# Kernel optimization log

Hardware: AMD Instinct MI355X
Metric: run time of the kernel (lower is better)

Reference implementation:

```python
import jax, jax.numpy as jnp
import numpy as np

N_NODES, N_EDGES, MAX_LEN, OB_DIM, HEADS = 4000, 64000, 64, 4, 1
IN_CH = MAX_LEN * OB_DIM          # 256
OUT_CH = MAX_LEN * OB_DIM         # 256
PE_DIM = 16                        # map_weights (heads*16) + p_t (16) cat -> 32


def setup_inputs() -> dict:
    key = jax.random.key(0)
    ks = jax.random.split(key, 8)
    x = jax.random.normal(ks[0], (N_NODES, IN_CH), dtype=jnp.float32)
    p_t = jax.random.normal(ks[1], (MAX_LEN, PE_DIM), dtype=jnp.float32)
    edge_index = jax.random.randint(ks[2], (2, N_EDGES), 0, N_NODES, dtype=jnp.int64)
    edge_weights = jax.random.uniform(ks[3], (N_EDGES,), dtype=jnp.float32)
    # learned params (torch Linear stored transposed: y = x @ W + b)
    s = 1.0 / np.sqrt(IN_CH)
    W_value = jax.random.uniform(ks[4], (IN_CH, HEADS * OUT_CH), jnp.float32, -s, s)
    b_value = jnp.zeros((HEADS * OUT_CH,), jnp.float32)
    W_inc = jax.random.uniform(ks[5], (IN_CH, HEADS * OUT_CH * 8), jnp.float32, -s, s)
    b_inc = jnp.zeros((HEADS * OUT_CH * 8,), jnp.float32)
    map_weights = jax.random.normal(ks[6], (N_NODES, HEADS * 16), jnp.float32) * 0.1
    return {"x": x, "p_t": p_t, "edge_index": edge_index, "edge_weights": edge_weights,
            "W_value": W_value, "b_value": b_value, "W_inc": W_inc, "b_inc": b_inc,
            "map_weights": map_weights}


def _segment_softmax(vals, index, num_segments):
    # PyG softmax: per-destination-segment, columnwise, with 1e-16 in denom
    seg_max = jax.ops.segment_max(vals, index, num_segments=num_segments)
    ex = jnp.exp(vals - seg_max[index])
    seg_sum = jax.ops.segment_sum(ex, index, num_segments=num_segments)
    return ex / (seg_sum[index] + 1e-16)


def reference(x, p_t, edge_index, edge_weights, W_value, b_value, W_inc, b_inc, map_weights):
    N = x.shape[0]
    E = edge_index.shape[1]
    L = p_t.shape[0]                      # n_step
    dst = edge_index[1]
    x_i = x[dst]                          # [E, IN_CH] gather of target-node feats
    # beta scoring (use_beta=True path)
    h_W = (x_i @ W_inc + b_inc).reshape(E, L, 32)
    w_v = map_weights[dst][:, None, :]    # [E, 1, 16]
    aa = jnp.concatenate([jnp.broadcast_to(w_v, (E, L, w_v.shape[-1])),
                          jnp.broadcast_to(p_t[None], (E, L, p_t.shape[-1]))], axis=-1)
    beta = jnp.mean(h_W * aa, axis=-1)    # [E, L]
    gamma = beta * edge_weights[:, None]  # [E, L]
    gamma = jnp.repeat(gamma, OB_DIM, axis=-1)   # [E, L*OB_DIM] == [E, HEADS*OUT_CH]
    all_edge_weights = jnp.mean(gamma, axis=1)   # [E]
    K = E // 2
    _, top_idx = jax.lax.top_k(all_edge_weights, K)
    gamma = gamma[top_idx]
    ei = edge_index[:, top_idx]
    index = ei[0]                          # faithful: original reassigns index = edge_index[0]
    x_i = x_i[top_idx]
    # segment softmax + weighted value aggregation
    gamma = _segment_softmax(gamma, index, N)
    out = jax.nn.relu(x_i @ W_value + b_value).reshape(K, HEADS, OUT_CH)
    out = out * gamma.reshape(K, HEADS, OUT_CH)
    out = jax.ops.segment_sum(out, index, num_segments=N)   # scatter-add aggregate
    return out.reshape(N, HEADS * OUT_CH)   # concat=True
```

## Files before the change

kernel.cpp:

```cpp
#include <hip/hip_runtime.h>
#include <stdint.h>

#define NN   4000
#define EE   64000
#define KSEL 32000
#define CAP  64

typedef __attribute__((ext_vector_type(8))) short bf16x8;
typedef __attribute__((ext_vector_type(4))) float f32x4;

static constexpr size_t O_HIST1 = 0;
static constexpr size_t O_HIST2 = 16384;
static constexpr size_t O_META  = 32768;
static constexpr size_t O_CNT   = 33024;
static constexpr size_t ZERO_BYTES = 49024;
static constexpr size_t O_BUCK  = 49024;
static constexpr size_t O_KEYS  = 1073024;
static constexpr size_t O_CAND  = 1585024;
static constexpr size_t O_CAND2 = 1841024;
static constexpr size_t O_MEANB = 2097024;
static constexpr size_t O_BMAT  = 2129024;
static constexpr size_t O_V     = 3153024;
static constexpr size_t O_WALLT = 5201024;
static constexpr size_t O_WVT   = 5758080;
static constexpr size_t O_WST   = 5889152;
static constexpr size_t O_BS1   = 5923968;
static constexpr size_t O_CB    = 5924096;
static constexpr size_t O_CONST = 5924352;

__device__ __forceinline__ unsigned short f2b(float f) {
  union { float f; unsigned u; } v; v.f = f;
  const unsigned r = v.u + 0x7fffu + ((v.u >> 16) & 1u);
  return (unsigned short)(r >> 16);
}
__device__ __forceinline__ float b2f(unsigned short b) {
  return __uint_as_float(((unsigned)b) << 16);
}
__device__ __forceinline__ bf16x8 ld_cvt8(const float* __restrict__ p) {
  const float4 fa = *(const float4*)p;
  const float4 fb = *(const float4*)(p + 4);
  bf16x8 r;
  r[0] = (short)f2b(fa.x); r[1] = (short)f2b(fa.y);
  r[2] = (short)f2b(fa.z); r[3] = (short)f2b(fa.w);
  r[4] = (short)f2b(fb.x); r[5] = (short)f2b(fb.y);
  r[6] = (short)f2b(fb.z); r[7] = (short)f2b(fb.w);
  return r;
}

__device__ __forceinline__ void block_select(const unsigned* __restrict__ hist,
                                             unsigned target, unsigned* sh,
                                             unsigned& pbin, unsigned& rem) {
  const int t = threadIdx.x;
  unsigned h[16];
  unsigned s = 0;
#pragma unroll
  for (int b = 0; b < 16; ++b) { h[b] = hist[t * 16 + b]; s += h[b]; }
  sh[t] = s;
  __syncthreads();
  for (int off = 1; off < 256; off <<= 1) {
    const unsigned a = (t + off < 256) ? sh[t + off] : 0u;
    __syncthreads();
    sh[t] += a;
    __syncthreads();
  }
  const unsigned mysuf = sh[t];
  const unsigned sufnext = (t < 255) ? sh[t + 1] : 0u;
  __syncthreads();
  if (mysuf >= target && sufnext < target) {
    unsigned cum = sufnext;
#pragma unroll
    for (int b = 15; b >= 0; --b) {
      const unsigned hv = h[b];
      if (cum + hv >= target) { sh[256] = (unsigned)(t * 16 + b); sh[257] = target - cum; break; }
      cum += hv;
    }
  }
  __syncthreads();
  pbin = sh[256]; rem = sh[257];
  __syncthreads();
}

__global__ void rk_prep(const float* __restrict__ W_inc, const float* __restrict__ p_t,
                        const float* __restrict__ b_inc, const float* __restrict__ W_value,
                        unsigned short* __restrict__ Wallt, unsigned short* __restrict__ Wvt,
                        double* __restrict__ WsT,
                        double* __restrict__ bs1, float* __restrict__ cb,
                        double* __restrict__ consts, unsigned* __restrict__ zws) {
  const int i = blockIdx.x;
  const int l = threadIdx.x;
  const int gid = i * 64 + l;
  if (gid < (int)(ZERO_BYTES / 4)) zws[gid] = 0u;
  __shared__ double sred[64];
  const int base = i * 2048 + l * 32;
#pragma unroll
  for (int c = 0; c < 16; ++c)
    Wallt[(size_t)(l * 16 + c) * 256 + i] = f2b(W_inc[base + c]);
  double accP = 0.0;
#pragma unroll
  for (int c = 0; c < 16; ++c)
    accP += (double)W_inc[base + 16 + c] * (double)p_t[l * 16 + c];
  Wallt[(size_t)(1024 + l) * 256 + i] = f2b((float)accP);
#pragma unroll
  for (int j = 0; j < 4; ++j)
    Wvt[(size_t)(l * 4 + j) * 256 + i] = f2b(W_value[i * 256 + l * 4 + j]);
  sred[l] = accP;
  __syncthreads();
  if (l == 0) {
    double s = 0.0;
    for (int j = 0; j < 64; ++j) s += sred[j];
    WsT[16 * 256 + i] = s;
  }
  if (l < 16) {
    double s = 0.0;
    for (int l2 = 0; l2 < 64; ++l2) s += (double)W_inc[i * 2048 + l2 * 32 + l];
    WsT[l * 256 + i] = s;
  }
  if (i == 0) {
    __syncthreads();
    if (l < 16) {
      double s = 0.0;
      for (int l2 = 0; l2 < 64; ++l2) s += (double)b_inc[l2 * 32 + l];
      bs1[l] = s;
    }
    double cbv = 0.0;
#pragma unroll
    for (int c = 0; c < 16; ++c)
      cbv += (double)p_t[l * 16 + c] * (double)b_inc[l * 32 + 16 + c];
    cb[l] = (float)cbv;
    sred[l] = cbv;
    __syncthreads();
    if (l == 0) {
      double s = 0.0;
      for (int j = 0; j < 64; ++j) s += sred[j];
      consts[0] = s;
    }
  }
}

__global__ __launch_bounds__(256) void rk_mbv(
    const float* __restrict__ x, const float* __restrict__ mw,
    const double* __restrict__ WsT,
    const double* __restrict__ bs1, const double* __restrict__ consts,
    double* __restrict__ meanB,
    const unsigned short* __restrict__ Wallt, const unsigned short* __restrict__ Wvt,
    const float* __restrict__ b_inc, const float* __restrict__ cb,
    const float* __restrict__ b_value,
    float* __restrict__ Bmat, unsigned short* __restrict__ V) {
  __shared__ double wst[17 * 256];
  const int bid = blockIdx.x;
  const int t = threadIdx.x;
  if (bid < 250) {
#pragma unroll
    for (int j = 0; j < 17; ++j) wst[j * 256 + t] = WsT[j * 256 + t];
    __syncthreads();
    const int lt = t & 63;
    const int w = t >> 6;
#pragma unroll
    for (int nn = 0; nn < 4; ++nn) {
      const int n = bid * 16 + w * 4 + nn;
      double mwv[16];
#pragma unroll
      for (int c = 0; c < 16; ++c) mwv[c] = (double)mw[n * 16 + c];
      double acc = 0.0;
#pragma unroll
      for (int rep = 0; rep < 4; ++rep) {
        const int i = lt + rep * 64;
        double weff = wst[16 * 256 + i];
#pragma unroll
        for (int c = 0; c < 16; ++c) weff += mwv[c] * wst[c * 256 + i];
        acc += (double)x[n * 256 + i] * weff;
      }
      for (int off = 32; off > 0; off >>= 1) acc += __shfl_down(acc, off, 64);
      if (lt == 0) {
        double s = acc + consts[0];
#pragma unroll
        for (int c = 0; c < 16; ++c) s += mwv[c] * bs1[c];
        meanB[n] = s * (1.0 / 2048.0);
      }
    }
  } else {
    const int b2 = bid - 250;
    const int wv = t >> 6, lane = t & 63;
    const int lr = lane & 15, kg = lane >> 4;
    const int n0 = (b2 % 125) * 32;
    const int by = b2 / 125;
    const int l0 = by * 16;
    const int c0 = by * 64 + wv * 16;
    f32x4 acc[2][5] = {};
    f32x4 accv[2] = {};
    const float* ax0 = x + (size_t)(n0 + lr) * 256 + kg * 8;
    const float* ax1 = ax0 + 16 * 256;
    const unsigned short* bp[5];
#pragma unroll
    for (int j = 0; j < 4; ++j)
      bp[j] = Wallt + (size_t)((l0 + wv * 4 + j) * 16 + lr) * 256 + kg * 8;
    bp[4] = Wallt + (size_t)(1024 + l0 + lr) * 256 + kg * 8;
    const unsigned short* bpv = Wvt + (size_t)(c0 + lr) * 256 + kg * 8;
#pragma unroll
    for (int kk = 0; kk < 8; ++kk) {
      const bf16x8 a0 = ld_cvt8(ax0 + kk * 32);
      const bf16x8 a1 = ld_cvt8(ax1 + kk * 32);
#pragma unroll
      for (int j = 0; j < 5; ++j) {
        const bf16x8 b = *(const bf16x8*)(bp[j] + kk * 32);
        acc[0][j] = __builtin_amdgcn_mfma_f32_16x16x32_bf16(a0, b, acc[0][j], 0, 0, 0);
        acc[1][j] = __builtin_amdgcn_mfma_f32_16x16x32_bf16(a1, b, acc[1][j], 0, 0, 0);
      }
      const bf16x8 bv = *(const bf16x8*)(bpv + kk * 32);
      accv[0] = __builtin_amdgcn_mfma_f32_16x16x32_bf16(a0, bv, accv[0], 0, 0, 0);
      accv[1] = __builtin_amdgcn_mfma_f32_16x16x32_bf16(a1, bv, accv[1], 0, 0, 0);
    }
    const int c = lr, rg = kg;
#pragma unroll
    for (int rt = 0; rt < 2; ++rt) {
      const int rbase = n0 + rt * 16 + rg * 4;
      float mwv[4];
#pragma unroll
      for (int r = 0; r < 4; ++r) mwv[r] = mw[(rbase + r) * 16 + c];
#pragma unroll
      for (int j = 0; j < 4; ++j) {
        const int lj = l0 + wv * 4 + j;
        const float bi = b_inc[lj * 32 + c];
        const float cbl = cb[lj];
#pragma unroll
        for (int r = 0; r < 4; ++r) {
          float prod = (acc[rt][j][r] + bi) * mwv[r];
#pragma unroll
          for (int off = 1; off < 16; off <<= 1) prod += __shfl_xor(prod, off, 64);
          const float c2 = __shfl(acc[rt][4][r], (lane & 48) | (wv * 4 + j), 64);
          if (c == 0) Bmat[(rbase + r) * 64 + lj] = (prod + c2 + cbl) * (1.0f / 32.0f);
        }
      }
    }
    const float bv = b_value[c0 + c];
#pragma unroll
    for (int rt = 0; rt < 2; ++rt)
#pragma unroll
      for (int r = 0; r < 4; ++r) {
        const float val = fmaxf(accv[rt][r] + bv, 0.f);
        V[(size_t)(n0 + rt * 16 + rg * 4 + r) * 256 + c0 + c] = f2b(val);
      }
  }
}

__global__ void rk_keys(const int* __restrict__ ei, const float* __restrict__ ew,
                        const double* __restrict__ meanB,
                        unsigned long long* __restrict__ keys, unsigned* __restrict__ hist1) {
  __shared__ unsigned lh[4096];
  const int t = threadIdx.x;
#pragma unroll
  for (int i = 0; i < 16; ++i) lh[t + i * 256] = 0u;
  __syncthreads();
  const int e = blockIdx.x * 256 + t;
  const int dst = ei[EE + e];
  const double aew = (double)ew[e] * meanB[dst];
  const unsigned long long b = (unsigned long long)__double_as_longlong(aew);
  const unsigned long long s = (b & 0x8000000000000000ull) ? ~b : (b | 0x8000000000000000ull);
  keys[e] = s;
  atomicAdd(&lh[(unsigned)(s >> 52)], 1u);
  __syncthreads();
#pragma unroll
  for (int i = 0; i < 16; ++i) {
    const unsigned v = lh[t + i * 256];
    if (v) atomicAdd(&hist1[t + i * 256], v);
  }
}

__global__ void rk_mark1(const unsigned long long* __restrict__ keys, const int* __restrict__ ei,
                         unsigned* __restrict__ meta, int* __restrict__ cand,
                         unsigned* __restrict__ cnt, int* __restrict__ bucket,
                         const unsigned* __restrict__ hist1, unsigned* __restrict__ hist2) {
  __shared__ unsigned sh[258];
  unsigned p1, m1;
  block_select(hist1, (unsigned)KSEL, sh, p1, m1);
  if (blockIdx.x == 0 && threadIdx.x == 0) { meta[0] = p1; meta[1] = m1; }
  const int e = blockIdx.x * 256 + threadIdx.x;
  const unsigned long long k = keys[e];
  const unsigned b12 = (unsigned)(k >> 52);
  if (b12 > p1) {
    const int src = ei[e];
    const unsigned pos = atomicAdd(&cnt[src], 1u);
    bucket[src * CAP + pos] = e;
  } else if (b12 == p1) {
    const unsigned pos = atomicAdd(&meta[2], 1u);
    cand[pos] = e;
    atomicAdd(&hist2[(unsigned)(k >> 40) & 0xFFFu], 1u);
  }
}

__global__ __launch_bounds__(1024) void rk_m2t(
    const unsigned long long* __restrict__ keys, const int* __restrict__ ei,
    unsigned* __restrict__ meta, const int* __restrict__ cand,
    int* __restrict__ cand2, unsigned* __restrict__ cnt, int* __restrict__ bucket,
    const unsigned* __restrict__ hist2) {
  __shared__ unsigned suf[1024];
  __shared__ unsigned sp[2];
  const int t = threadIdx.x;
  const unsigned m1 = meta[1];
  unsigned h[4];
  unsigned s = 0;
#pragma unroll
  for (int b = 0; b < 4; ++b) { h[b] = hist2[t * 4 + b]; s += h[b]; }
  suf[t] = s;
  __syncthreads();
  for (int off = 1; off < 1024; off <<= 1) {
    const unsigned a = (t + off < 1024) ? suf[t + off] : 0u;
    __syncthreads();
    suf[t] += a;
    __syncthreads();
  }
  const unsigned mysuf = suf[t];
  const unsigned sufnext = (t < 1023) ? suf[t + 1] : 0u;
  if (mysuf >= m1 && sufnext < m1) {
    unsigned cum = sufnext;
#pragma unroll
    for (int b = 3; b >= 0; --b) {
      const unsigned hv = h[b];
      if (cum + hv >= m1) { sp[0] = (unsigned)(t * 4 + b); sp[1] = m1 - cum; break; }
      cum += hv;
    }
  }
  __syncthreads();
  const unsigned p2 = sp[0], m2 = sp[1];
  const int C1 = (int)meta[2];
  for (int i = t; i < C1; i += 1024) {
    const int e = cand[i];
    const unsigned d12 = (unsigned)(keys[e] >> 40) & 0xFFFu;
    if (d12 > p2) {
      const int src = ei[e];
      const unsigned pos = atomicAdd(&cnt[src], 1u);
      bucket[src * CAP + pos] = e;
    } else if (d12 == p2) {
      const unsigned pos = atomicAdd(&meta[3], 1u);
      cand2[pos] = e;
    }
  }
  __threadfence();
  __syncthreads();
  const int C2 = (int)__hip_atomic_load(&meta[3], __ATOMIC_ACQUIRE, __HIP_MEMORY_SCOPE_AGENT);
  for (int i = t; i < C2; i += 1024) {
    const int e_i = cand2[i];
    const unsigned long long k_i = keys[e_i];
    int r = 0;
    for (int j = 0; j < C2; ++j) {
      const int e_j = cand2[j];
      const unsigned long long k_j = keys[e_j];
      if (k_j > k_i || (k_j == k_i && e_j < e_i)) ++r;
    }
    if (r < (int)m2) {
      const int src = ei[e_i];
      const unsigned pos = atomicAdd(&cnt[src], 1u);
      bucket[src * CAP + pos] = e_i;
    }
  }
}

__global__ void rk_out(const int* __restrict__ ei, const float* __restrict__ ew,
                       const unsigned* __restrict__ cnt, const int* __restrict__ bucket,
                       const float* __restrict__ Bmat, const unsigned short* __restrict__ V,
                       float* __restrict__ out) {
  const int n = blockIdx.x;
  const int t = threadIdx.x;
  const int l = t >> 2;
  __shared__ int   sdst[CAP];
  __shared__ float sew[CAP];
  const unsigned d = cnt[n];
  if (t < (int)d) {
    const int e = bucket[n * CAP + t];
    sdst[t] = ei[EE + e];
    sew[t] = ew[e];
  }
  __syncthreads();
  float s = 0.f, acc = 0.f;
  for (unsigned i = 0; i < d; ++i) {
    const int dst = sdst[i];
    const float p = __expf(Bmat[dst * 64 + l] * sew[i]);
    s += p;
    acc += p * b2f(V[(size_t)dst * 256 + t]);
  }
  out[(size_t)n * 256 + t] = acc / (s + 1e-16f);
}

extern "C" void kernel_launch(void* const* d_in, const int* in_sizes, int n_in,
                              void* d_out, int out_size, void* d_ws, size_t ws_size,
                              hipStream_t stream) {
  const float* x       = (const float*)d_in[0];
  const float* p_t     = (const float*)d_in[1];
  const int*   ei      = (const int*)d_in[2];
  const float* ew      = (const float*)d_in[3];
  const float* W_value = (const float*)d_in[4];
  const float* b_value = (const float*)d_in[5];
  const float* W_inc   = (const float*)d_in[6];
  const float* b_inc   = (const float*)d_in[7];
  const float* mw      = (const float*)d_in[8];
  float* out = (float*)d_out;
  char* ws = (char*)d_ws;

  unsigned*           hist1 = (unsigned*)(ws + O_HIST1);
  unsigned*           hist2 = (unsigned*)(ws + O_HIST2);
  unsigned*           meta  = (unsigned*)(ws + O_META);
  unsigned*           cnt   = (unsigned*)(ws + O_CNT);
  int*                buck  = (int*)(ws + O_BUCK);
  unsigned long long* keys  = (unsigned long long*)(ws + O_KEYS);
  int*                cand  = (int*)(ws + O_CAND);
  int*                cand2 = (int*)(ws + O_CAND2);
  double*             meanB = (double*)(ws + O_MEANB);
  float*              Bmat  = (float*)(ws + O_BMAT);
  unsigned short*     V     = (unsigned short*)(ws + O_V);
  unsigned short*     Wallt = (unsigned short*)(ws + O_WALLT);
  unsigned short*     Wvt   = (unsigned short*)(ws + O_WVT);
  double*             WsT   = (double*)(ws + O_WST);
  double*             bs1   = (double*)(ws + O_BS1);
  float*              cb    = (float*)(ws + O_CB);
  double*             cst   = (double*)(ws + O_CONST);

  rk_prep<<<256, 64, 0, stream>>>(W_inc, p_t, b_inc, W_value, Wallt, Wvt,
                                  WsT, bs1, cb, cst, (unsigned*)ws);
  rk_mbv<<<750, 256, 0, stream>>>(x, mw, WsT, bs1, cst, meanB,
                                  Wallt, Wvt, b_inc, cb, b_value, Bmat, V);
  rk_keys<<<250, 256, 0, stream>>>(ei, ew, meanB, keys, hist1);
  rk_mark1<<<250, 256, 0, stream>>>(keys, ei, meta, cand, cnt, buck, hist1, hist2);
  rk_m2t<<<1, 1024, 0, stream>>>(keys, ei, meta, cand, cand2, cnt, buck, hist2);
  rk_out<<<NN, 256, 0, stream>>>(ei, ew, cnt, buck, Bmat, V, out);
}
```

Before: 74.63 us.

## Split fused meanB/Bmat kernel into two separate launches

The combined rk_mbv kernel, which branched by block index between an FP64 meanB reduction and an MFMA GEMM for Bmat and V, is split into two kernels. The meanB kernel now handles one node per wave across 1000 blocks instead of four per wave, preloads x, and breaks the 16-term FP64 dot product into four independent accumulators to shorten the dependency chain. Separating the kernels lets each be compiled with its own register and LDS budget rather than the union of both paths. The cost is an extra launch and serialization between the two kernels, which previously ran concurrently within one grid.

New measurement: 76.79 us. 2.9% more time.

```diff
diff --git a/kernel.cpp b/kernel.cpp
--- a/kernel.cpp
+++ b/kernel.cpp
@@ -137,110 +137,114 @@
   }
 }
 
-__global__ __launch_bounds__(256) void rk_mbv(
+__global__ __launch_bounds__(256) void rk_meanB(
     const float* __restrict__ x, const float* __restrict__ mw,
-    const double* __restrict__ WsT,
-    const double* __restrict__ bs1, const double* __restrict__ consts,
-    double* __restrict__ meanB,
+    const double* __restrict__ WsT, const double* __restrict__ bs1,
+    const double* __restrict__ consts, double* __restrict__ meanB) {
+  __shared__ double wst[17 * 256];
+  const int t = threadIdx.x;
+#pragma unroll
+  for (int j = 0; j < 17; ++j) wst[j * 256 + t] = WsT[j * 256 + t];
+  __syncthreads();
+  const int lt = t & 63;
+  const int n = blockIdx.x * 4 + (t >> 6);
+  float xv[4];
+#pragma unroll
+  for (int rep = 0; rep < 4; ++rep) xv[rep] = x[n * 256 + lt + rep * 64];
+  double mwv[16];
+#pragma unroll
+  for (int c = 0; c < 16; ++c) mwv[c] = (double)mw[n * 16 + c];
+  double acc = 0.0;
+#pragma unroll
+  for (int rep = 0; rep < 4; ++rep) {
+    const int i = lt + rep * 64;
+    double wa0 = wst[16 * 256 + i], wa1 = 0.0, wa2 = 0.0, wa3 = 0.0;
+#pragma unroll
+    for (int c = 0; c < 16; c += 4) {
+      wa0 += mwv[c + 0] * wst[(c + 0) * 256 + i];
+      wa1 += mwv[c + 1] * wst[(c + 1) * 256 + i];
+      wa2 += mwv[c + 2] * wst[(c + 2) * 256 + i];
+      wa3 += mwv[c + 3] * wst[(c + 3) * 256 + i];
+    }
+    acc += (double)xv[rep] * ((wa0 + wa1) + (wa2 + wa3));
+  }
+  for (int off = 32; off > 0; off >>= 1) acc += __shfl_down(acc, off, 64);
+  if (lt == 0) {
+    double s = acc + consts[0];
+#pragma unroll
+    for (int c = 0; c < 16; ++c) s += mwv[c] * bs1[c];
+    meanB[n] = s * (1.0 / 2048.0);
+  }
+}
+
+__global__ __launch_bounds__(256) void rk_bmatv(
+    const float* __restrict__ x, const float* __restrict__ mw,
     const unsigned short* __restrict__ Wallt, const unsigned short* __restrict__ Wvt,
     const float* __restrict__ b_inc, const float* __restrict__ cb,
     const float* __restrict__ b_value,
     float* __restrict__ Bmat, unsigned short* __restrict__ V) {
-  __shared__ double wst[17 * 256];
-  const int bid = blockIdx.x;
-  const int t = threadIdx.x;
-  if (bid < 250) {
-#pragma unroll
-    for (int j = 0; j < 17; ++j) wst[j * 256 + t] = WsT[j * 256 + t];
-    __syncthreads();
-    const int lt = t & 63;
-    const int w = t >> 6;
-#pragma unroll
-    for (int nn = 0; nn < 4; ++nn) {
-      const int n = bid * 16 + w * 4 + nn;
-      double mwv[16];
-#pragma unroll
-      for (int c = 0; c < 16; ++c) mwv[c] = (double)mw[n * 16 + c];
-      double acc = 0.0;
-#pragma unroll
-      for (int rep = 0; rep < 4; ++rep) {
-        const int i = lt + rep * 64;
-        double weff = wst[16 * 256 + i];
-#pragma unroll
-        for (int c = 0; c < 16; ++c) weff += mwv[c] * wst[c * 256 + i];
-        acc += (double)x[n * 256 + i] * weff;
+  const int t = threadIdx.x;
+  const int b2 = blockIdx.x;
+  const int wv = t >> 6, lane = t & 63;
+  const int lr = lane & 15, kg = lane >> 4;
+  const int n0 = (b2 % 125) * 32;
+  const int by = b2 / 125;
+  const int l0 = by * 16;
+  const int c0 = by * 64 + wv * 16;
+  f32x4 acc[2][5] = {};
+  f32x4 accv[2] = {};
+  const float* ax0 = x + (size_t)(n0 + lr) * 256 + kg * 8;
+  const float* ax1 = ax0 + 16 * 256;
+  const unsigned short* bp[5];
+#pragma unroll
+  for (int j = 0; j < 4; ++j)
+    bp[j] = Wallt + (size_t)((l0 + wv * 4 + j) * 16 + lr) * 256 + kg * 8;
+  bp[4] = Wallt + (size_t)(1024 + l0 + lr) * 256 + kg * 8;
+  const unsigned short* bpv = Wvt + (size_t)(c0 + lr) * 256 + kg * 8;
+#pragma unroll
+  for (int kk = 0; kk < 8; ++kk) {
+    const bf16x8 a0 = ld_cvt8(ax0 + kk * 32);
+    const bf16x8 a1 = ld_cvt8(ax1 + kk * 32);
+#pragma unroll
+    for (int j = 0; j < 5; ++j) {
+      const bf16x8 b = *(const bf16x8*)(bp[j] + kk * 32);
+      acc[0][j] = __builtin_amdgcn_mfma_f32_16x16x32_bf16(a0, b, acc[0][j], 0, 0, 0);
+      acc[1][j] = __builtin_amdgcn_mfma_f32_16x16x32_bf16(a1, b, acc[1][j], 0, 0, 0);
+    }
+    const bf16x8 bv = *(const bf16x8*)(bpv + kk * 32);
+    accv[0] = __builtin_amdgcn_mfma_f32_16x16x32_bf16(a0, bv, accv[0], 0, 0, 0);
+    accv[1] = __builtin_amdgcn_mfma_f32_16x16x32_bf16(a1, bv, accv[1], 0, 0, 0);
+  }
+  const int c = lr, rg = kg;
+#pragma unroll
+  for (int rt = 0; rt < 2; ++rt) {
+    const int rbase = n0 + rt * 16 + rg * 4;
+    float mwv[4];
+#pragma unroll
+    for (int r = 0; r < 4; ++r) mwv[r] = mw[(rbase + r) * 16 + c];
+#pragma unroll
+    for (int j = 0; j < 4; ++j) {
+      const int lj = l0 + wv * 4 + j;
+      const float bi = b_inc[lj * 32 + c];
+      const float cbl = cb[lj];
+#pragma unroll
+      for (int r = 0; r < 4; ++r) {
+        float prod = (acc[rt][j][r] + bi) * mwv[r];
+#pragma unroll
+        for (int off = 1; off < 16; off <<= 1) prod += __shfl_xor(prod, off, 64);
+        const float c2 = __shfl(acc[rt][4][r], (lane & 48) | (wv * 4 + j), 64);
+        if (c == 0) Bmat[(rbase + r) * 64 + lj] = (prod + c2 + cbl) * (1.0f / 32.0f);
       }
-      for (int off = 32; off > 0; off >>= 1) acc += __shfl_down(acc, off, 64);
-      if (lt == 0) {
-        double s = acc + consts[0];
-#pragma unroll
-        for (int c = 0; c < 16; ++c) s += mwv[c] * bs1[c];
-        meanB[n] = s * (1.0 / 2048.0);
-      }
-    }
-  } else {
-    const int b2 = bid - 250;
-    const int wv = t >> 6, lane = t & 63;
-    const int lr = lane & 15, kg = lane >> 4;
-    const int n0 = (b2 % 125) * 32;
-    const int by = b2 / 125;
-    const int l0 = by * 16;
-    const int c0 = by * 64 + wv * 16;
-    f32x4 acc[2][5] = {};
-    f32x4 accv[2] = {};
-    const float* ax0 = x + (size_t)(n0 + lr) * 256 + kg * 8;
-    const float* ax1 = ax0 + 16 * 256;
-    const unsigned short* bp[5];
-#pragma unroll
-    for (int j = 0; j < 4; ++j)
-      bp[j] = Wallt + (size_t)((l0 + wv * 4 + j) * 16 + lr) * 256 + kg * 8;
-    bp[4] = Wallt + (size_t)(1024 + l0 + lr) * 256 + kg * 8;
-    const unsigned short* bpv = Wvt + (size_t)(c0 + lr) * 256 + kg * 8;
-#pragma unroll
-    for (int kk = 0; kk < 8; ++kk) {
-      const bf16x8 a0 = ld_cvt8(ax0 + kk * 32);
-      const bf16x8 a1 = ld_cvt8(ax1 + kk * 32);
-#pragma unroll
-      for (int j = 0; j < 5; ++j) {
-        const bf16x8 b = *(const bf16x8*)(bp[j] + kk * 32);
-        acc[0][j] = __builtin_amdgcn_mfma_f32_16x16x32_bf16(a0, b, acc[0][j], 0, 0, 0);
-        acc[1][j] = __builtin_amdgcn_mfma_f32_16x16x32_bf16(a1, b, acc[1][j], 0, 0, 0);
-      }
-      const bf16x8 bv = *(const bf16x8*)(bpv + kk * 32);
-      accv[0] = __builtin_amdgcn_mfma_f32_16x16x32_bf16(a0, bv, accv[0], 0, 0, 0);
-      accv[1] = __builtin_amdgcn_mfma_f32_16x16x32_bf16(a1, bv, accv[1], 0, 0, 0);
-    }
-    const int c = lr, rg = kg;
-#pragma unroll
-    for (int rt = 0; rt < 2; ++rt) {
-      const int rbase = n0 + rt * 16 + rg * 4;
-      float mwv[4];
-#pragma unroll
-      for (int r = 0; r < 4; ++r) mwv[r] = mw[(rbase + r) * 16 + c];
-#pragma unroll
-      for (int j = 0; j < 4; ++j) {
-        const int lj = l0 + wv * 4 + j;
-        const float bi = b_inc[lj * 32 + c];
-        const float cbl = cb[lj];
-#pragma unroll
-        for (int r = 0; r < 4; ++r) {
-          float prod = (acc[rt][j][r] + bi) * mwv[r];
-#pragma unroll
-          for (int off = 1; off < 16; off <<= 1) prod += __shfl_xor(prod, off, 64);
-          const float c2 = __shfl(acc[rt][4][r], (lane & 48) | (wv * 4 + j), 64);
-          if (c == 0) Bmat[(rbase + r) * 64 + lj] = (prod + c2 + cbl) * (1.0f / 32.0f);
-        }
-      }
-    }
-    const float bv = b_value[c0 + c];
-#pragma unroll
-    for (int rt = 0; rt < 2; ++rt)
-#pragma unroll
-      for (int r = 0; r < 4; ++r) {
-        const float val = fmaxf(accv[rt][r] + bv, 0.f);
-        V[(size_t)(n0 + rt * 16 + rg * 4 + r) * 256 + c0 + c] = f2b(val);
-      }
-  }
+    }
+  }
+  const float bv = b_value[c0 + c];
+#pragma unroll
+  for (int rt = 0; rt < 2; ++rt)
+#pragma unroll
+    for (int r = 0; r < 4; ++r) {
+      const float val = fmaxf(accv[rt][r] + bv, 0.f);
+      V[(size_t)(n0 + rt * 16 + rg * 4 + r) * 256 + c0 + c] = f2b(val);
+    }
 }
 
 __global__ void rk_keys(const int* __restrict__ ei, const float* __restrict__ ew,
@@ -416,8 +420,8 @@
 
   rk_prep<<<256, 64, 0, stream>>>(W_inc, p_t, b_inc, W_value, Wallt, Wvt,
                                   WsT, bs1, cb, cst, (unsigned*)ws);
-  rk_mbv<<<750, 256, 0, stream>>>(x, mw, WsT, bs1, cst, meanB,
-                                  Wallt, Wvt, b_inc, cb, b_value, Bmat, V);
+  rk_meanB<<<1000, 256, 0, stream>>>(x, mw, WsT, bs1, cst, meanB);
+  rk_bmatv<<<500, 256, 0, stream>>>(x, mw, Wallt, Wvt, b_inc, cb, b_value, Bmat, V);
   rk_keys<<<250, 256, 0, stream>>>(ei, ew, meanB, keys, hist1);
   rk_mark1<<<250, 256, 0, stream>>>(keys, ei, meta, cand, cnt, buck, hist1, hist2);
   rk_m2t<<<1, 1024, 0, stream>>>(keys, ei, meta, cand, cand2, cnt, buck, hist2);
```
